# Kernel optimization log

Hardware: AMD Instinct MI355X
Metric: run time of the kernel (lower is better)

Reference implementation:

```python
import jax, jax.numpy as jnp
import numpy as np

C = 512
C8 = C // 8  # query/key projection dim


def _conv1x1(x, W, b):
    # x: [B,C,H,W], W: [O,C], b: [O] -> [B,O,H,W]
    return jnp.einsum('bchw,oc->bohw', x, W) + b[None, :, None, None]


def setup_inputs() -> dict:
    key = jax.random.key(0)
    ks = jax.random.split(key, 13)
    B, H, Wd = 4, 64, 64
    s = 0.02
    return {
        'x_rgb': jax.random.normal(ks[0], (B, C, H, Wd), jnp.float32),
        'x_dep': jax.random.normal(ks[1], (B, C, H, Wd), jnp.float32),
        'Wq': jax.random.normal(ks[2], (C8, C), jnp.float32) * s,
        'bq': jnp.zeros((C8,), jnp.float32),
        'Wk': jax.random.normal(ks[3], (C8, C), jnp.float32) * s,
        'bk': jnp.zeros((C8,), jnp.float32),
        'Wdq': jax.random.normal(ks[4], (C8, C), jnp.float32) * s,
        'bdq': jnp.zeros((C8,), jnp.float32),
        'Wdk': jax.random.normal(ks[5], (C8, C), jnp.float32) * s,
        'bdk': jnp.zeros((C8,), jnp.float32),
        'Wv': jax.random.normal(ks[6], (C, C), jnp.float32) * s,
        'bv': jnp.zeros((C,), jnp.float32),
        'gamma': jnp.zeros((1,), jnp.float32),
    }


def reference(x_rgb, x_dep, Wq, bq, Wk, bk, Wdq, bdq, Wdk, bdk, Wv, bv, gamma):
    B, Cc, H, Wd = x_rgb.shape
    N = H * Wd
    # 1x1 conv projections, flattened over spatial positions -> [B, c, N]
    q = _conv1x1(x_rgb, Wq, bq).reshape(B, C8, N)
    k = _conv1x1(x_rgb, Wk, bk).reshape(B, C8, N)
    qd = _conv1x1(x_dep, Wdq, bdq).reshape(B, C8, N)
    kd = _conv1x1(x_dep, Wdk, bdk).reshape(B, C8, N)
    # fused dual-stream energy: [B, N, N]
    energy = jnp.einsum('bci,bcj->bij', q, k) + jnp.einsum('bci,bcj->bij', qd, kd)
    attention = jax.nn.softmax(energy, axis=-1)
    v = _conv1x1(x_rgb, Wv, bv).reshape(B, Cc, N)
    # out[b,c,i] = sum_j v[b,c,j] * attention[b,i,j]
    out = jnp.einsum('bcj,bij->bci', v, attention).reshape(B, Cc, H, Wd)
    return gamma[0] * out + x_rgb
```

## Files before the change

kernel.cpp:

```cpp
#include <hip/hip_runtime.h>
#include <math.h>

#define B_ 4
#define C_ 512
#define D_ 128
#define N_ 4096

typedef short s4v __attribute__((ext_vector_type(4)));
typedef short s8v __attribute__((ext_vector_type(8)));
typedef float f4v __attribute__((ext_vector_type(4)));

__device__ __forceinline__ unsigned short f2bf(float x) {
    union { float f; unsigned u; } v; v.f = x;
    unsigned r = v.u + 0x7FFF + ((v.u >> 16) & 1);
    return (unsigned short)(r >> 16);
}
__device__ __forceinline__ float bf2f(unsigned short h) {
    union { unsigned u; float f; } v; v.u = ((unsigned)h) << 16; return v.f;
}

__global__ __launch_bounds__(256) void cvt_w_kernel(
    const float* __restrict__ Wq,  const float* __restrict__ bq,
    const float* __restrict__ Wk,  const float* __restrict__ bk,
    const float* __restrict__ Wdq, const float* __restrict__ bdq,
    const float* __restrict__ Wdk, const float* __restrict__ bdk,
    const float* __restrict__ Wv,  const float* __restrict__ bv,
    unsigned short* __restrict__ Wb, float* __restrict__ biasb)
{
    int t = blockIdx.x * 256 + threadIdx.x;
    int e0 = t * 8;
    int row = e0 >> 9, c = e0 & 511;
    const float* src; int r0;
    if (row < 64)       { src = Wq;  r0 = row; }
    else if (row < 128) { src = Wk;  r0 = row - 64; }
    else if (row < 640) { src = Wv;  r0 = row - 128; }
    else if (row < 704) { src = Wdq; r0 = row - 640; }
    else                { src = Wdk; r0 = row - 704; }
    const float* p = src + (size_t)r0 * 512 + c;
    s8v o;
    #pragma unroll
    for (int u = 0; u < 8; ++u) ((unsigned short*)&o)[u] = f2bf(p[u]);
    *(s8v*)&Wb[e0] = o;
    if (blockIdx.x == 0) {
        #pragma unroll
        for (int s = 0; s < 3; ++s) {
            int o2 = threadIdx.x + 256 * s;
            float v;
            if (o2 < 64)       v = bq[o2];
            else if (o2 < 128) v = bk[o2 - 64];
            else if (o2 < 640) v = bv[o2 - 128];
            else if (o2 < 704) v = bdq[o2 - 640];
            else               v = bdk[o2 - 704];
            biasb[o2] = v;
        }
    }
}

__global__ __launch_bounds__(256) void xpose_kernel(
    const float* __restrict__ x_rgb, const float* __restrict__ x_dep,
    unsigned short* __restrict__ Xt)
{
    __shared__ __align__(16) unsigned short Ls[64 * 72];
    const int cT = blockIdx.x & 7, iT = blockIdx.x >> 3;
    const int b = blockIdx.y, st = blockIdx.z;
    const int t = threadIdx.x;
    const float* Xb = (st ? x_dep : x_rgb) + (size_t)b * C_ * N_;

    const int c4 = t >> 4, i4 = t & 15;
    {
        const float* xp = Xb + (size_t)(cT * 64 + c4 * 4) * N_ + iT * 64 + i4 * 4;
        float4 r0 = *(const float4*)(xp);
        float4 r1 = *(const float4*)(xp + N_);
        float4 r2 = *(const float4*)(xp + 2 * N_);
        float4 r3 = *(const float4*)(xp + 3 * N_);
        s4v p0 = { (short)f2bf(r0.x), (short)f2bf(r1.x), (short)f2bf(r2.x), (short)f2bf(r3.x) };
        s4v p1 = { (short)f2bf(r0.y), (short)f2bf(r1.y), (short)f2bf(r2.y), (short)f2bf(r3.y) };
        s4v p2 = { (short)f2bf(r0.z), (short)f2bf(r1.z), (short)f2bf(r2.z), (short)f2bf(r3.z) };
        s4v p3 = { (short)f2bf(r0.w), (short)f2bf(r1.w), (short)f2bf(r2.w), (short)f2bf(r3.w) };
        *(s4v*)&Ls[(i4 * 4 + 0) * 72 + c4 * 4] = p0;
        *(s4v*)&Ls[(i4 * 4 + 1) * 72 + c4 * 4] = p1;
        *(s4v*)&Ls[(i4 * 4 + 2) * 72 + c4 * 4] = p2;
        *(s4v*)&Ls[(i4 * 4 + 3) * 72 + c4 * 4] = p3;
    }
    __syncthreads();
    unsigned short* dst = Xt + ((size_t)(st * 4 + b) * N_ + iT * 64) * 512 + cT * 64;
    #pragma unroll
    for (int s = 0; s < 2; ++s) {
        int lin = t + 256 * s;
        int row = lin >> 3, g = lin & 7;
        *(s8v*)&dst[(size_t)row * 512 + g * 8] = *(const s8v*)&Ls[row * 72 + g * 8];
    }
}

__global__ __launch_bounds__(256) void gemm_kernel(
    const unsigned short* __restrict__ Wb, const float* __restrict__ biasb,
    const unsigned short* __restrict__ Xt,
    unsigned short* __restrict__ Q, unsigned short* __restrict__ K,
    unsigned short* __restrict__ V)
{
    __shared__ __align__(16) unsigned short Ws[128 * 64];
    __shared__ __align__(16) unsigned short Xs[128 * 64];
    const int b  = blockIdx.x >> 5;
    const int i0 = (blockIdx.x & 31) * 128;
    const int by = blockIdx.y;
    const int mbase = by * 128;
    const int st = (by == 5);
    const int t = threadIdx.x, w = t >> 6;
    const int lane = t & 63, col = lane & 15, quad = lane >> 4;
    const int mh = (w & 1) * 64, nh = (w >> 1) * 64;

    const unsigned short* Wg = Wb + (size_t)mbase * 512;
    const unsigned short* Xg = Xt + ((size_t)(st * 4 + b) * N_ + i0) * 512;

    f4v acc[4][4];
    #pragma unroll
    for (int mt = 0; mt < 4; ++mt)
        #pragma unroll
        for (int nt = 0; nt < 4; ++nt) acc[mt][nt] = (f4v){0.f, 0.f, 0.f, 0.f};

    for (int kc = 0; kc < 8; ++kc) {
        const int k0 = kc * 64;
        s8v wt[4], xt[4];
        #pragma unroll
        for (int s = 0; s < 4; ++s) {
            int lin = t + 256 * s;
            int row = lin >> 3, g = lin & 7;
            wt[s] = *(const s8v*)&Wg[(size_t)row * 512 + k0 + g * 8];
            xt[s] = *(const s8v*)&Xg[(size_t)row * 512 + k0 + g * 8];
        }
        __syncthreads();
        #pragma unroll
        for (int s = 0; s < 4; ++s) {
            int lin = t + 256 * s;
            int row = lin >> 3, g = lin & 7;
            int soff = row * 64 + ((g ^ (row & 7)) * 8);
            *(s8v*)&Ws[soff] = wt[s];
            *(s8v*)&Xs[soff] = xt[s];
        }
        __syncthreads();
        #pragma unroll
        for (int kk = 0; kk < 2; ++kk) {
            const int gq = kk * 4 + quad;
            s8v af[4], bf[4];
            #pragma unroll
            for (int mt = 0; mt < 4; ++mt) {
                int r = mh + mt * 16 + col;
                af[mt] = *(const s8v*)&Ws[r * 64 + ((gq ^ (r & 7)) * 8)];
            }
            #pragma unroll
            for (int nt = 0; nt < 4; ++nt) {
                int r = nh + nt * 16 + col;
                bf[nt] = *(const s8v*)&Xs[r * 64 + ((gq ^ (r & 7)) * 8)];
            }
            #pragma unroll
            for (int nt = 0; nt < 4; ++nt)
                #pragma unroll
                for (int mt = 0; mt < 4; ++mt)
                    acc[mt][nt] = __builtin_amdgcn_mfma_f32_16x16x32_bf16(
                        af[mt], bf[nt], acc[mt][nt], 0, 0, 0);
        }
    }

    const int mlo0 = mbase + mh;
    #pragma unroll
    for (int mt = 0; mt < 4; ++mt) {
        const int mlo = mlo0 + mt * 16;
        f4v bi = *(const f4v*)&biasb[mlo + quad * 4];
        if (mlo < 128 || mlo >= 640) {
            unsigned short* dst; int dbase;
            if (mlo < 64)       { dst = Q; dbase = mlo; }
            else if (mlo < 128) { dst = K; dbase = mlo - 64; }
            else if (mlo < 704) { dst = Q; dbase = 64 + (mlo - 640); }
            else                { dst = K; dbase = 64 + (mlo - 704); }
            #pragma unroll
            for (int nt = 0; nt < 4; ++nt) {
                int i = i0 + nh + nt * 16 + col;
                s4v pk = { (short)f2bf(acc[mt][nt][0] + bi[0]),
                           (short)f2bf(acc[mt][nt][1] + bi[1]),
                           (short)f2bf(acc[mt][nt][2] + bi[2]),
                           (short)f2bf(acc[mt][nt][3] + bi[3]) };
                *(s4v*)&dst[((size_t)b * N_ + i) * D_ + dbase + quad * 4] = pk;
            }
        } else {
            int c0 = mlo - 128 + quad * 4;
            #pragma unroll
            for (int nt = 0; nt < 4; ++nt) {
                int i = i0 + nh + nt * 16 + col;
                #pragma unroll
                for (int r = 0; r < 4; ++r)
                    V[((size_t)b * C_ + c0 + r) * N_ + i] =
                        f2bf(acc[mt][nt][r] + bi[r]);
            }
        }
    }
}

__global__ __launch_bounds__(256, 2) void attn_kernel(
    const unsigned short* __restrict__ Q, const unsigned short* __restrict__ K,
    const unsigned short* __restrict__ V,
    unsigned short* __restrict__ O_ws, float* __restrict__ l_ws)
{
    __shared__ __align__(16) unsigned short Ks[32 * 136];
    __shared__ __align__(16) unsigned short Ps[64 * 40];
    __shared__ __align__(16) unsigned short Vs[512 * 32];
    __shared__ float lred[2][64];

    const int id  = blockIdx.x;
    const int grp = id & 7;
    const int b   = grp & 3;
    const int jh  = grp >> 2;
    const int it  = id >> 3;
    const int i0  = it * 64;
    const int jb  = jh * 2048;
    const int t = threadIdx.x, w = t >> 6;
    const int lane = t & 63, col = lane & 15, quad = lane >> 4;
    const int ih = w & 1, jq = w >> 1;

    const unsigned short* Kg = K + (size_t)b * N_ * D_;
    const unsigned short* Vg = V + (size_t)b * C_ * N_;

    s8v qf[2][4];
    #pragma unroll
    for (int ig = 0; ig < 2; ++ig) {
        const unsigned short* qr =
            Q + ((size_t)b * N_ + i0 + ih * 32 + ig * 16 + col) * D_ + quad * 8;
        #pragma unroll
        for (int kk = 0; kk < 4; ++kk) qf[ig][kk] = *(const s8v*)(qr + kk * 32);
    }

    f4v accO[4][8];
    #pragma unroll
    for (int rt = 0; rt < 4; ++rt)
        #pragma unroll
        for (int ct = 0; ct < 8; ++ct) accO[rt][ct] = (f4v){0.f, 0.f, 0.f, 0.f};
    float lsum[2] = {0.f, 0.f};

    for (int tt = 0; tt < 64; ++tt) {
        const int j0 = jb + tt * 32;
        s8v kt[2], vt[8];
        #pragma unroll
        for (int s = 0; s < 2; ++s) {
            int gi = t + 256 * s;
            kt[s] = *(const s8v*)&Kg[(size_t)(j0 + (gi >> 4)) * D_ + (gi & 15) * 8];
        }
        #pragma unroll
        for (int s = 0; s < 8; ++s) {
            int gi = t + 256 * s;
            vt[s] = *(const s8v*)&Vg[(size_t)(gi >> 2) * N_ + j0 + (gi & 3) * 8];
        }
        asm volatile("s_waitcnt lgkmcnt(0)" ::: "memory");
        __builtin_amdgcn_s_barrier();
        #pragma unroll
        for (int s = 0; s < 2; ++s) {
            int gi = t + 256 * s;
            *(s8v*)&Ks[(gi >> 4) * 136 + (gi & 15) * 8] = kt[s];
        }
        asm volatile("s_waitcnt lgkmcnt(0)" ::: "memory");
        __builtin_amdgcn_s_barrier();
        f4v s0 = (f4v){0.f, 0.f, 0.f, 0.f};
        f4v s1 = (f4v){0.f, 0.f, 0.f, 0.f};
        #pragma unroll
        for (int kk = 0; kk < 4; ++kk) {
            s8v kf = *(const s8v*)&Ks[(jq * 16 + col) * 136 + kk * 32 + quad * 8];
            s0 = __builtin_amdgcn_mfma_f32_16x16x32_bf16(kf, qf[0][kk], s0, 0, 0, 0);
            s1 = __builtin_amdgcn_mfma_f32_16x16x32_bf16(kf, qf[1][kk], s1, 0, 0, 0);
        }
        #pragma unroll
        for (int ig = 0; ig < 2; ++ig) {
            f4v sv = ig ? s1 : s0;
            s4v p; float ls = 0.f;
            #pragma unroll
            for (int r = 0; r < 4; ++r) {
                float e = __expf(sv[r]);
                ls += e;
                p[r] = (short)f2bf(e);
            }
            lsum[ig] += ls;
            *(s4v*)&Ps[(ih * 32 + ig * 16 + col) * 40 + jq * 16 + quad * 4] = p;
        }
        #pragma unroll
        for (int s = 0; s < 8; ++s) {
            int gi = t + 256 * s;
            int c = gi >> 2, g = gi & 3;
            int sw = (g + c + (c >> 2)) & 3;
            *(s8v*)&Vs[c * 32 + sw * 8] = vt[s];
        }
        asm volatile("s_waitcnt lgkmcnt(0)" ::: "memory");
        __builtin_amdgcn_s_barrier();
        s8v pf[4];
        #pragma unroll
        for (int rt = 0; rt < 4; ++rt)
            pf[rt] = *(const s8v*)&Ps[(rt * 16 + col) * 40 + quad * 8];
        __builtin_amdgcn_s_setprio(1);
        #pragma unroll
        for (int ct = 0; ct < 8; ++ct) {
            int row = w * 128 + ct * 16 + col;
            int sw = (quad + row + (row >> 2)) & 3;
            s8v vf = *(const s8v*)&Vs[row * 32 + sw * 8];
            #pragma unroll
            for (int rt = 0; rt < 4; ++rt)
                accO[rt][ct] = __builtin_amdgcn_mfma_f32_16x16x32_bf16(pf[rt], vf, accO[rt][ct], 0, 0, 0);
        }
        __builtin_amdgcn_s_setprio(0);
    }

    #pragma unroll
    for (int ig = 0; ig < 2; ++ig) {
        float v = lsum[ig];
        v += __shfl_xor(v, 16);
        v += __shfl_xor(v, 32);
        if (quad == 0) lred[jq][ih * 32 + ig * 16 + col] = v;
    }
    __syncthreads();
    if (t < 64)
        l_ws[((size_t)jh * B_ + b) * N_ + i0 + t] = lred[0][t] + lred[1][t];

    const size_t wbase =
        ((((size_t)jh * B_ + b) * 64 + it) * 4 + w) * 8192;
    #pragma unroll
    for (int ct = 0; ct < 8; ++ct)
        #pragma unroll
        for (int rt = 0; rt < 4; ++rt) {
            s4v pk = { (short)f2bf(accO[rt][ct][0]), (short)f2bf(accO[rt][ct][1]),
                       (short)f2bf(accO[rt][ct][2]), (short)f2bf(accO[rt][ct][3]) };
            *(s4v*)&O_ws[wbase + (size_t)(ct * 4 + rt) * 256 + lane * 4] = pk;
        }
}

__global__ __launch_bounds__(256) void combine_kernel(
    const unsigned short* __restrict__ O_ws, const float* __restrict__ l_ws,
    const float* __restrict__ x_rgb, const float* __restrict__ gamma,
    float* __restrict__ out)
{
    const size_t half = (size_t)B_ * 64 * 4 * 8192;
    const int bx = blockIdx.x;
    const int ct = bx & 7;
    const int w  = (bx >> 3) & 3;
    const int it = (bx >> 5) & 63;
    const int b  = bx >> 11;
    const int t  = threadIdx.x;
    const int rt = t >> 6, l = t & 63;
    const int c_sub = l >> 2, qd = l & 3;

    const int c = w * 128 + ct * 16 + c_sub;
    const int i = it * 64 + rt * 16 + qd * 4;

    const size_t seg = (((size_t)b * 64 + it) * 4 + w) * 8192
                     + (size_t)(ct * 4 + rt) * 256 + (qd * 16 + c_sub) * 4;
    s4v o0 = *(const s4v*)&O_ws[seg];
    s4v o1 = *(const s4v*)&O_ws[half + seg];
    float4 l0 = *(const float4*)&l_ws[(size_t)b * N_ + i];
    float4 l1 = *(const float4*)&l_ws[(size_t)(B_ + b) * N_ + i];
    size_t base = ((size_t)b * C_ + c) * N_ + i;
    float4 x4 = *(const float4*)&x_rgb[base];
    float g = gamma[0];
    float4 r;
    r.x = g * (bf2f((unsigned short)o0[0]) + bf2f((unsigned short)o1[0])) / (l0.x + l1.x) + x4.x;
    r.y = g * (bf2f((unsigned short)o0[1]) + bf2f((unsigned short)o1[1])) / (l0.y + l1.y) + x4.y;
    r.z = g * (bf2f((unsigned short)o0[2]) + bf2f((unsigned short)o1[2])) / (l0.z + l1.z) + x4.z;
    r.w = g * (bf2f((unsigned short)o0[3]) + bf2f((unsigned short)o1[3])) / (l0.w + l1.w) + x4.w;
    *(float4*)&out[base] = r;
}

extern "C" void kernel_launch(void* const* d_in, const int* in_sizes, int n_in,
                              void* d_out, int out_size, void* d_ws, size_t ws_size,
                              hipStream_t stream) {
    (void)in_sizes; (void)n_in; (void)out_size; (void)ws_size;
    const float* x_rgb = (const float*)d_in[0];
    const float* x_dep = (const float*)d_in[1];
    const float* Wq    = (const float*)d_in[2];
    const float* bq    = (const float*)d_in[3];
    const float* Wk    = (const float*)d_in[4];
    const float* bk    = (const float*)d_in[5];
    const float* Wdq   = (const float*)d_in[6];
    const float* bdq   = (const float*)d_in[7];
    const float* Wdk   = (const float*)d_in[8];
    const float* bdk   = (const float*)d_in[9];
    const float* Wv    = (const float*)d_in[10];
    const float* bv    = (const float*)d_in[11];
    const float* gamma = (const float*)d_in[12];
    float* out = (float*)d_out;

    unsigned short* Q     = (unsigned short*)d_ws;
    unsigned short* K     = Q + (size_t)B_ * N_ * D_;
    unsigned short* V     = K + (size_t)B_ * N_ * D_;
    unsigned short* Wb    = V + (size_t)B_ * C_ * N_;
    float*          biasb = (float*)(Wb + 768 * 512);
    unsigned short* XtO   = (unsigned short*)(biasb + 1024);
    float*          l_ws  = (float*)(XtO + (size_t)2 * B_ * C_ * N_);

    cvt_w_kernel<<<dim3(192), 256, 0, stream>>>(
        Wq, bq, Wk, bk, Wdq, bdq, Wdk, bdk, Wv, bv, Wb, biasb);
    xpose_kernel<<<dim3(512, 4, 2), 256, 0, stream>>>(x_rgb, x_dep, XtO);
    gemm_kernel<<<dim3(128, 6), 256, 0, stream>>>(Wb, biasb, XtO, Q, K, V);
    attn_kernel<<<dim3(512), 256, 0, stream>>>(Q, K, V, XtO, l_ws);
    combine_kernel<<<dim3(8192), 256, 0, stream>>>(XtO, l_ws, x_rgb, gamma, out);
}
```

Measured before the change: 280.0 us.

## Prefetch next K-chunk in projection GEMM and remap blocks for XCD locality

The projection GEMM now loads the next 64-wide K-chunk of W and X into registers while the current chunk is consumed from shared memory, so global latency overlaps the MFMA work. It also switches to a 1D grid that puts the six M-tiles of one (batch, position) X tile on the same XCD, so the shared X rows are reused from that XCD's L2. The change adds register pressure from keeping the prefetched values live and uses raw s_barrier with lgkmcnt waits. The GEMM is only a small part of the total next to the attention kernel.

```diff
diff --git a/kernel.cpp b/kernel.cpp
--- a/kernel.cpp
+++ b/kernel.cpp
@@ -100,9 +100,13 @@
 {
     __shared__ __align__(16) unsigned short Ws[128 * 64];
     __shared__ __align__(16) unsigned short Xs[128 * 64];
-    const int b  = blockIdx.x >> 5;
-    const int i0 = (blockIdx.x & 31) * 128;
-    const int by = blockIdx.y;
+    const int id  = blockIdx.x;
+    const int xcd = id & 7;
+    const int r   = id >> 3;
+    const int by  = r % 6;
+    const int grp = xcd + 8 * (r / 6);
+    const int b   = grp >> 5;
+    const int i0  = (grp & 31) * 128;
     const int mbase = by * 128;
     const int st = (by == 5);
     const int t = threadIdx.x, w = t >> 6;
@@ -118,17 +122,18 @@
         #pragma unroll
         for (int nt = 0; nt < 4; ++nt) acc[mt][nt] = (f4v){0.f, 0.f, 0.f, 0.f};
 
+    s8v wt[4], xt[4];
+    #pragma unroll
+    for (int s = 0; s < 4; ++s) {
+        int lin = t + 256 * s;
+        int row = lin >> 3, g = lin & 7;
+        wt[s] = *(const s8v*)&Wg[(size_t)row * 512 + g * 8];
+        xt[s] = *(const s8v*)&Xg[(size_t)row * 512 + g * 8];
+    }
+
     for (int kc = 0; kc < 8; ++kc) {
-        const int k0 = kc * 64;
-        s8v wt[4], xt[4];
-        #pragma unroll
-        for (int s = 0; s < 4; ++s) {
-            int lin = t + 256 * s;
-            int row = lin >> 3, g = lin & 7;
-            wt[s] = *(const s8v*)&Wg[(size_t)row * 512 + k0 + g * 8];
-            xt[s] = *(const s8v*)&Xg[(size_t)row * 512 + k0 + g * 8];
-        }
-        __syncthreads();
+        asm volatile("s_waitcnt lgkmcnt(0)" ::: "memory");
+        __builtin_amdgcn_s_barrier();
         #pragma unroll
         for (int s = 0; s < 4; ++s) {
             int lin = t + 256 * s;
@@ -137,20 +142,31 @@
             *(s8v*)&Ws[soff] = wt[s];
             *(s8v*)&Xs[soff] = xt[s];
         }
-        __syncthreads();
+        if (kc < 7) {
+            const int k1 = (kc + 1) * 64;
+            #pragma unroll
+            for (int s = 0; s < 4; ++s) {
+                int lin = t + 256 * s;
+                int row = lin >> 3, g = lin & 7;
+                wt[s] = *(const s8v*)&Wg[(size_t)row * 512 + k1 + g * 8];
+                xt[s] = *(const s8v*)&Xg[(size_t)row * 512 + k1 + g * 8];
+            }
+        }
+        asm volatile("s_waitcnt lgkmcnt(0)" ::: "memory");
+        __builtin_amdgcn_s_barrier();
         #pragma unroll
         for (int kk = 0; kk < 2; ++kk) {
             const int gq = kk * 4 + quad;
             s8v af[4], bf[4];
             #pragma unroll
             for (int mt = 0; mt < 4; ++mt) {
-                int r = mh + mt * 16 + col;
-                af[mt] = *(const s8v*)&Ws[r * 64 + ((gq ^ (r & 7)) * 8)];
+                int rr = mh + mt * 16 + col;
+                af[mt] = *(const s8v*)&Ws[rr * 64 + ((gq ^ (rr & 7)) * 8)];
             }
             #pragma unroll
             for (int nt = 0; nt < 4; ++nt) {
-                int r = nh + nt * 16 + col;
-                bf[nt] = *(const s8v*)&Xs[r * 64 + ((gq ^ (r & 7)) * 8)];
+                int rr = nh + nt * 16 + col;
+                bf[nt] = *(const s8v*)&Xs[rr * 64 + ((gq ^ (rr & 7)) * 8)];
             }
             #pragma unroll
             for (int nt = 0; nt < 4; ++nt)
@@ -187,9 +203,9 @@
             for (int nt = 0; nt < 4; ++nt) {
                 int i = i0 + nh + nt * 16 + col;
                 #pragma unroll
-                for (int r = 0; r < 4; ++r)
-                    V[((size_t)b * C_ + c0 + r) * N_ + i] =
-                        f2bf(acc[mt][nt][r] + bi[r]);
+                for (int rr = 0; rr < 4; ++rr)
+                    V[((size_t)b * C_ + c0 + rr) * N_ + i] =
+                        f2bf(acc[mt][nt][rr] + bi[rr]);
             }
         }
     }
@@ -392,7 +408,7 @@
     cvt_w_kernel<<<dim3(192), 256, 0, stream>>>(
         Wq, bq, Wk, bk, Wdq, bdq, Wdk, bdk, Wv, bv, Wb, biasb);
     xpose_kernel<<<dim3(512, 4, 2), 256, 0, stream>>>(x_rgb, x_dep, XtO);
-    gemm_kernel<<<dim3(128, 6), 256, 0, stream>>>(Wb, biasb, XtO, Q, K, V);
+    gemm_kernel<<<dim3(768), 256, 0, stream>>>(Wb, biasb, XtO, Q, K, V);
     attn_kernel<<<dim3(512), 256, 0, stream>>>(Q, K, V, XtO, l_ws);
     combine_kernel<<<dim3(8192), 256, 0, stream>>>(XtO, l_ws, x_rgb, gamma, out);
 }
```

Measured after the change: 289.8 us. 1.03x slower.
